# Kernel optimization log

Measured on AMD Instinct MI355X. Metric: run time of the kernel, lower is better.

Reference implementation:

```python
import jax, jax.numpy as jnp
import numpy as np

N_NODES = 50000
N_EDGES = 600000
DIM = 128
K = 3
N_LAYERS = 3
LEAKY_SLOPE = 0.01  # nn.LeakyReLU default
RE_NORM = 1.0       # 2/lambda_max with lambda_max=2 (standard ChebNet approximation)


def setup_inputs() -> dict:
    key = jax.random.key(0)
    ks = jax.random.split(key, 8)
    weights = jax.random.normal(ks[0], (N_NODES,), dtype=jnp.float32)
    src = jax.random.randint(ks[1], (N_EDGES,), 0, N_NODES)
    dst = jax.random.randint(ks[2], (N_EDGES,), 0, N_NODES)
    lin_in_w = jax.random.normal(ks[3], (1, DIM), dtype=jnp.float32) * 0.5
    lin_in_b = jnp.zeros((DIM,), dtype=jnp.float32)
    cheb_ws = jax.random.normal(ks[4], (N_LAYERS, K * DIM, DIM), dtype=jnp.float32) * 0.05
    cheb_bs = jnp.zeros((N_LAYERS, DIM), dtype=jnp.float32)
    pred_w = jax.random.normal(ks[5], (DIM, 1), dtype=jnp.float32) * 0.05
    pred_b = jnp.zeros((1,), dtype=jnp.float32)
    return {"weights": weights, "src": src, "dst": dst,
            "lin_in_w": lin_in_w, "lin_in_b": lin_in_b,
            "cheb_ws": cheb_ws, "cheb_bs": cheb_bs,
            "pred_w": pred_w, "pred_b": pred_b}


def _cheb_conv(x, W, b, src, dst, d_invsqrt, n):
    # DGL ChebConv with lambda_max=2 -> re_norm=1: scaled Laplacian L_hat = -D^-1/2 A D^-1/2
    def spmm(f):  # unnormalized Laplacian-style aggregation: D^-1/2 A D^-1/2 f
        h = f * d_invsqrt
        agg = jax.ops.segment_sum(h[src], dst, num_segments=n)
        return agg * d_invsqrt

    X0 = x
    terms = [X0]
    h = spmm(X0)
    X1 = -RE_NORM * h + X0 * (RE_NORM - 1.0)
    terms.append(X1)
    for _ in range(2, K):
        h = spmm(X1)
        Xi = -2.0 * RE_NORM * h + X1 * (2.0 * (RE_NORM - 1.0)) - X0
        terms.append(Xi)
        X0, X1 = X1, Xi
    Xt = jnp.concatenate(terms, axis=1)  # [N, K*DIM]
    return jax.nn.relu(Xt @ W + b)       # DGL ChebConv default activation=F.relu


def reference(weights, src, dst, lin_in_w, lin_in_b, cheb_ws, cheb_bs, pred_w, pred_b):
    n = weights.shape[0]
    # dgl.add_self_loop
    loop = jnp.arange(n, dtype=src.dtype)
    src_f = jnp.concatenate([src, loop])
    dst_f = jnp.concatenate([dst, loop])
    # in-degree normalization D^-1/2 (clamp min 1)
    deg = jax.ops.segment_sum(jnp.ones_like(dst_f, dtype=jnp.float32), dst_f, num_segments=n)
    d_invsqrt = jnp.power(jnp.clip(deg, 1.0), -0.5)[:, None]  # [N,1]

    feat = weights[:, None] @ lin_in_w + lin_in_b             # [N, DIM]
    emb = _cheb_conv(feat, cheb_ws[0], cheb_bs[0], src_f, dst_f, d_invsqrt, n)
    for i in range(1, N_LAYERS):
        emb = jax.nn.leaky_relu(emb, negative_slope=LEAKY_SLOPE)
        emb = _cheb_conv(emb, cheb_ws[i], cheb_bs[i], src_f, dst_f, d_invsqrt, n)
    logits = emb @ pred_w + pred_b                            # do_train=True path
    return logits
```

## Files before the change

### kernel.cpp

```cpp
#include <hip/hip_runtime.h>

typedef unsigned int uint;
typedef unsigned short ushort;

#define NN 50000
#define NE 600000
#define DIM 128
#define KD 384
#define PADK 40

typedef __attribute__((ext_vector_type(8))) short short8;
typedef __attribute__((ext_vector_type(4))) float float4v;

static __device__ __forceinline__ ushort f2b(float f) {
    uint u = __float_as_uint(f);
    return (ushort)((u + 0x7FFFu + ((u >> 16) & 1u)) >> 16);
}
static __device__ __forceinline__ float blo(uint u) { return __uint_as_float(u << 16); }
static __device__ __forceinline__ float bhi(uint u) { return __uint_as_float(u & 0xFFFF0000u); }

__global__ void k_init(int* __restrict__ cnt, const float* __restrict__ cw,
                       ushort* __restrict__ wt) {
    if (blockIdx.x < 49) {
        int i = blockIdx.x * 256 + threadIdx.x;
        if (i < 12544) ((int4*)cnt)[i] = make_int4(0, 0, 0, 0);
    } else {
        int i = (blockIdx.x - 49) * 256 + threadIdx.x;
        if (i < 3 * KD * DIM) {
            int l = i / (KD * DIM), rem = i - l * (KD * DIM);
            int k = rem >> 7, n = rem & 127;
            wt[(size_t)l * KD * DIM + (size_t)n * KD + k] = f2b(cw[i]);
        }
    }
}

__global__ void k_hist(const int* __restrict__ dst, int* __restrict__ cnt) {
    int e = blockIdx.x * 256 + threadIdx.x;
    if (e < NE) atomicAdd(&cnt[dst[e]], 1);
}

__global__ __launch_bounds__(256) void k_scan1(const int* __restrict__ cnt,
                                               int* __restrict__ incl,
                                               int* __restrict__ bsums,
                                               float* __restrict__ dinv) {
    __shared__ int sh[256];
    int i = blockIdx.x * 256 + threadIdx.x;
    int v = (i < NN) ? cnt[i] : 0;
    if (i < NN) dinv[i] = rsqrtf((float)(v + 1));
    sh[threadIdx.x] = v;
    __syncthreads();
    for (int d = 1; d < 256; d <<= 1) {
        int t = (threadIdx.x >= d) ? sh[threadIdx.x - d] : 0;
        __syncthreads();
        sh[threadIdx.x] += t;
        __syncthreads();
    }
    incl[i] = sh[threadIdx.x];
    if (threadIdx.x == 255) bsums[blockIdx.x] = sh[255];
}

__global__ __launch_bounds__(256) void k_scan3(const int* __restrict__ cnt,
                                               int* __restrict__ incl_cursor,
                                               const int* __restrict__ bsums,
                                               int* __restrict__ offs) {
    __shared__ int sh[256];
    __shared__ int boff;
    int tid = threadIdx.x;
    int v = (tid < 196) ? bsums[tid] : 0;
    sh[tid] = v;
    __syncthreads();
    for (int d = 1; d < 256; d <<= 1) {
        int t = (tid >= d) ? sh[tid - d] : 0;
        __syncthreads();
        sh[tid] += t;
        __syncthreads();
    }
    if (tid == blockIdx.x) boff = sh[tid] - v;
    __syncthreads();
    int i = blockIdx.x * 256 + tid;
    if (i >= NN) return;
    int excl = incl_cursor[i] - cnt[i] + boff;
    offs[i] = excl;
    incl_cursor[i] = excl;
    if (i == NN - 1) offs[NN] = NE;
}

__global__ void k_fill(const int* __restrict__ src, const int* __restrict__ dst,
                       int* __restrict__ cursor, const float* __restrict__ dinv,
                       const float* __restrict__ w_in,
                       uint2* __restrict__ csrE, float* __restrict__ hw) {
    int e = blockIdx.x * 256 + threadIdx.x;
    if (e < NE) {
        int s = src[e], d = dst[e];
        int p = atomicAdd(&cursor[d], 1);
        float ds = dinv[s];
        uint2 rec;
        rec.x = (uint)s;
        rec.y = __float_as_uint(ds * dinv[d]);
        csrE[p] = rec;
        hw[p] = ds * w_in[s];
    }
}

__global__ __launch_bounds__(256) void k_gather1_l1(
        const float* __restrict__ w, const float* __restrict__ lw,
        const float* __restrict__ lb, const int* __restrict__ offs,
        const uint2* __restrict__ csrE, const float* __restrict__ hw,
        const float* __restrict__ dinv,
        ushort* __restrict__ Qb, ushort* __restrict__ Pb) {
    int n = blockIdx.x * 4 + (threadIdx.x >> 6);
    int lane = threadIdx.x & 63;
    int j0 = offs[n], j1 = offs[n + 1];
    float dn = dinv[n];
    float sA = 0.f, sB = 0.f;
    const float* ew = (const float*)csrE;
    for (int j = j0 + lane; j < j1; j += 64) {
        sA += hw[j];
        sB += ew[2 * j + 1];
    }
#pragma unroll
    for (int off = 32; off > 0; off >>= 1) {
        sA += __shfl_down(sA, off, 64);
        sB += __shfl_down(sB, off, 64);
    }
    sA = __shfl(sA, 0, 64) * dn;
    sB = __shfl(sB, 0, 64);
    float id = dn * dn;
    float wn = w[n];
    float lw0 = lw[2 * lane], lw1 = lw[2 * lane + 1];
    float lb0 = lb[2 * lane], lb1 = lb[2 * lane + 1];
    float x0a = wn * lw0 + lb0, x0b = wn * lw1 + lb1;
    ushort2 pb2; pb2.x = f2b(x0a); pb2.y = f2b(x0b);
    ((ushort2*)(Pb + (size_t)n * DIM))[lane] = pb2;
    ushort2 ub;
    ub.x = f2b(-(sA * lw0 + sB * lb0 + x0a * id));
    ub.y = f2b(-(sA * lw1 + sB * lb1 + x0b * id));
    ((ushort2*)(Qb + (size_t)n * DIM))[lane] = ub;
}

__global__ __launch_bounds__(256) void k_gather1(
        const ushort* __restrict__ Xb, const int* __restrict__ offs,
        const uint2* __restrict__ csrE, const float* __restrict__ dinv,
        ushort* __restrict__ Qb) {
    int n = __builtin_amdgcn_readfirstlane(blockIdx.x * 4 + (threadIdx.x >> 6));
    int lane = threadIdx.x & 63;
    int j0 = offs[n], j1 = offs[n + 1];
    const uint* Xu = (const uint*)Xb;
    float a0 = 0.f, a1 = 0.f;
#pragma unroll 4
    for (int j = j0; j < j1; ++j) {
        uint2 e = csrE[j];
        float wv = __uint_as_float(e.y);
        uint u = Xu[(size_t)e.x * 64 + lane];
        a0 = fmaf(wv, blo(u), a0);
        a1 = fmaf(wv, bhi(u), a1);
    }
    float dn = dinv[n];
    float id = dn * dn;
    uint un = Xu[(size_t)n * 64 + lane];
    uint ow = (uint)f2b(-(a0 + blo(un) * id))
            | ((uint)f2b(-(a1 + bhi(un) * id)) << 16);
    ((uint*)Qb)[(size_t)n * 64 + lane] = ow;
}

__global__ __launch_bounds__(256) void k_gather2(
        const ushort* __restrict__ X1b, const ushort* __restrict__ X0b,
        const int* __restrict__ offs, const uint2* __restrict__ csrE,
        const float* __restrict__ dinv, ushort* __restrict__ Rb) {
    int n = __builtin_amdgcn_readfirstlane(blockIdx.x * 4 + (threadIdx.x >> 6));
    int lane = threadIdx.x & 63;
    int j0 = offs[n], j1 = offs[n + 1];
    const uint* Xu = (const uint*)X1b;
    float a0 = 0.f, a1 = 0.f;
#pragma unroll 4
    for (int j = j0; j < j1; ++j) {
        uint2 e = csrE[j];
        float wv = __uint_as_float(e.y);
        uint u = Xu[(size_t)e.x * 64 + lane];
        a0 = fmaf(wv, blo(u), a0);
        a1 = fmaf(wv, bhi(u), a1);
    }
    float dn = dinv[n];
    float id = dn * dn;
    uint u1n = Xu[(size_t)n * 64 + lane];
    uint u0n = ((const uint*)X0b)[(size_t)n * 64 + lane];
    uint ow = (uint)f2b(-2.f * (a0 + blo(u1n) * id) - blo(u0n))
            | ((uint)f2b(-2.f * (a1 + bhi(u1n) * id) - bhi(u0n)) << 16);
    ((uint*)Rb)[(size_t)n * 64 + lane] = ow;
}

__global__ __launch_bounds__(256) void k_gemm(
        const ushort* __restrict__ X0b, const ushort* __restrict__ X1b,
        const ushort* __restrict__ X2b, const ushort* __restrict__ Wt,
        const float* __restrict__ bias, ushort* __restrict__ outb) {
    __shared__ ushort As[128 * PADK];
    __shared__ ushort Bs[128 * PADK];
    int tid = threadIdx.x;
    int nbase = blockIdx.x * 128;
    int wave = tid >> 6, lane = tid & 63;
    int wr = wave >> 1, wc = wave & 1;
    int l15 = lane & 15, quad = lane >> 4;

    float4v acc[4][4];
#pragma unroll
    for (int i = 0; i < 4; ++i)
#pragma unroll
        for (int j = 0; j < 4; ++j) acc[i][j] = (float4v)0.f;

    int srow = tid >> 1, shalf = tid & 1;
    int gm = nbase + srow; if (gm >= NN) gm = NN - 1;

    for (int c = 0; c < 12; ++c) {
        int part = c >> 2;
        int k0 = (c & 3) * 32;
        const ushort* Xp = (part == 0) ? X0b : ((part == 1) ? X1b : X2b);
        const uint4* ga = (const uint4*)(Xp + (size_t)gm * DIM + k0 + shalf * 16);
        uint4 a0 = ga[0], a1 = ga[1];
        const uint4* gb = (const uint4*)(Wt + (size_t)srow * KD + c * 32 + shalf * 16);
        uint4 b0 = gb[0], b1 = gb[1];
        __syncthreads();
        uint4* pa = (uint4*)(As + srow * PADK + shalf * 16);
        pa[0] = a0; pa[1] = a1;
        uint4* pb = (uint4*)(Bs + srow * PADK + shalf * 16);
        pb[0] = b0; pb[1] = b1;
        __syncthreads();
        short8 af[4], bf[4];
#pragma unroll
        for (int i = 0; i < 4; ++i) {
            af[i] = *(const short8*)(As + (wr * 64 + i * 16 + l15) * PADK + quad * 8);
            bf[i] = *(const short8*)(Bs + (wc * 64 + i * 16 + l15) * PADK + quad * 8);
        }
#pragma unroll
        for (int i = 0; i < 4; ++i)
#pragma unroll
            for (int j = 0; j < 4; ++j)
                acc[i][j] = __builtin_amdgcn_mfma_f32_16x16x32_bf16(
                    af[i], bf[j], acc[i][j], 0, 0, 0);
    }

    float bv[4];
#pragma unroll
    for (int j = 0; j < 4; ++j) bv[j] = bias[wc * 64 + j * 16 + l15];
#pragma unroll
    for (int i = 0; i < 4; ++i) {
#pragma unroll
        for (int r = 0; r < 4; ++r) {
            int node = nbase + wr * 64 + i * 16 + quad * 4 + r;
            if (node < NN) {
#pragma unroll
                for (int j = 0; j < 4; ++j) {
                    int col = wc * 64 + j * 16 + l15;
                    outb[(size_t)node * DIM + col] =
                        f2b(fmaxf(acc[i][j][r] + bv[j], 0.f));
                }
            }
        }
    }
}

__global__ __launch_bounds__(256) void k_gemm_pred(
        const ushort* __restrict__ X0b, const ushort* __restrict__ X1b,
        const ushort* __restrict__ X2b, const ushort* __restrict__ Wt,
        const float* __restrict__ bias, const float* __restrict__ pw,
        const float* __restrict__ pb, float* __restrict__ logits) {
    __shared__ ushort As[128 * PADK];
    __shared__ ushort Bs[128 * PADK];
    __shared__ float lsum[128];
    int tid = threadIdx.x;
    int nbase = blockIdx.x * 128;
    int wave = tid >> 6, lane = tid & 63;
    int wr = wave >> 1, wc = wave & 1;
    int l15 = lane & 15, quad = lane >> 4;

    float4v acc[4][4];
#pragma unroll
    for (int i = 0; i < 4; ++i)
#pragma unroll
        for (int j = 0; j < 4; ++j) acc[i][j] = (float4v)0.f;

    int srow = tid >> 1, shalf = tid & 1;
    int gm = nbase + srow; if (gm >= NN) gm = NN - 1;

    for (int c = 0; c < 12; ++c) {
        int part = c >> 2;
        int k0 = (c & 3) * 32;
        const ushort* Xp = (part == 0) ? X0b : ((part == 1) ? X1b : X2b);
        const uint4* ga = (const uint4*)(Xp + (size_t)gm * DIM + k0 + shalf * 16);
        uint4 a0 = ga[0], a1 = ga[1];
        const uint4* gb = (const uint4*)(Wt + (size_t)srow * KD + c * 32 + shalf * 16);
        uint4 b0 = gb[0], b1 = gb[1];
        __syncthreads();
        uint4* pa = (uint4*)(As + srow * PADK + shalf * 16);
        pa[0] = a0; pa[1] = a1;
        uint4* pb2 = (uint4*)(Bs + srow * PADK + shalf * 16);
        pb2[0] = b0; pb2[1] = b1;
        __syncthreads();
        short8 af[4], bf[4];
#pragma unroll
        for (int i = 0; i < 4; ++i) {
            af[i] = *(const short8*)(As + (wr * 64 + i * 16 + l15) * PADK + quad * 8);
            bf[i] = *(const short8*)(Bs + (wc * 64 + i * 16 + l15) * PADK + quad * 8);
        }
#pragma unroll
        for (int i = 0; i < 4; ++i)
#pragma unroll
            for (int j = 0; j < 4; ++j)
                acc[i][j] = __builtin_amdgcn_mfma_f32_16x16x32_bf16(
                    af[i], bf[j], acc[i][j], 0, 0, 0);
    }

    __syncthreads();
    if (tid < 128) lsum[tid] = 0.f;
    __syncthreads();
    float bv[4], pwv[4];
#pragma unroll
    for (int j = 0; j < 4; ++j) {
        int col = wc * 64 + j * 16 + l15;
        bv[j] = bias[col];
        pwv[j] = pw[col];
    }
#pragma unroll
    for (int i = 0; i < 4; ++i) {
#pragma unroll
        for (int r = 0; r < 4; ++r) {
            float local = 0.f;
#pragma unroll
            for (int j = 0; j < 4; ++j)
                local = fmaf(fmaxf(acc[i][j][r] + bv[j], 0.f), pwv[j], local);
            local += __shfl_xor(local, 1, 64);
            local += __shfl_xor(local, 2, 64);
            local += __shfl_xor(local, 4, 64);
            local += __shfl_xor(local, 8, 64);
            if (l15 == 0)
                atomicAdd(&lsum[wr * 64 + i * 16 + quad * 4 + r], local);
        }
    }
    __syncthreads();
    if (tid < 128) {
        int node = nbase + tid;
        if (node < NN) logits[node] = lsum[tid] + pb[0];
    }
}

extern "C" void kernel_launch(void* const* d_in, const int* in_sizes, int n_in,
                              void* d_out, int out_size, void* d_ws, size_t ws_size,
                              hipStream_t stream) {
    int i_weights = 0, i_src = 1, i_dst = 2, i_lw = 3, i_lb = 4,
        i_cw = 5, i_cb = 6, i_pw = 7, i_pb = 8;
    {
        int seen600k = 0, seen128 = 0;
        for (int i = 0; i < n_in; ++i) {
            int s = in_sizes[i];
            if (s == 50000) i_weights = i;
            else if (s == 600000) { if (seen600k == 0) i_src = i; else i_dst = i; ++seen600k; }
            else if (s == 128) { if (seen128 == 0) i_lw = i; else if (seen128 == 1) i_lb = i; else i_pw = i; ++seen128; }
            else if (s == 147456) i_cw = i;
            else if (s == 384) i_cb = i;
            else if (s == 1) i_pb = i;
        }
    }
    const float* weights = (const float*)d_in[i_weights];
    const int*   src     = (const int*)d_in[i_src];
    const int*   dst     = (const int*)d_in[i_dst];
    const float* lin_w   = (const float*)d_in[i_lw];
    const float* lin_b   = (const float*)d_in[i_lb];
    const float* cheb_w  = (const float*)d_in[i_cw];
    const float* cheb_b  = (const float*)d_in[i_cb];
    const float* pred_w  = (const float*)d_in[i_pw];
    const float* pred_b  = (const float*)d_in[i_pb];
    float* out = (float*)d_out;

    float*  ws      = (float*)d_ws;
    float*  dinv    = ws;
    int*    offs    = (int*)(ws + 50048);
    int*    cnt     = offs + 50056;
    int*    incl    = cnt + 50176;
    int*    bsums   = incl + 50176;
    uint2*  csrE    = (uint2*)(bsums + 256);
    float*  hw      = (float*)(csrE + NE);
    ushort* Pb      = (ushort*)(hw + NE);
    ushort* Qb      = Pb + (size_t)NN * DIM;
    ushort* Rb      = Qb + (size_t)NN * DIM;
    ushort* Wtb     = Rb + (size_t)NN * DIM;

    k_init<<<625, 256, 0, stream>>>(cnt, cheb_w, Wtb);
    k_hist<<<2344, 256, 0, stream>>>(dst, cnt);
    k_scan1<<<196, 256, 0, stream>>>(cnt, incl, bsums, dinv);
    k_scan3<<<196, 256, 0, stream>>>(cnt, incl, bsums, offs);
    k_fill<<<2344, 256, 0, stream>>>(src, dst, incl, dinv, weights, csrE, hw);

    k_gather1_l1<<<12500, 256, 0, stream>>>(weights, lin_w, lin_b, offs, csrE,
                                            hw, dinv, Qb, Pb);
    k_gather2<<<12500, 256, 0, stream>>>(Qb, Pb, offs, csrE, dinv, Rb);
    k_gemm<<<391, 256, 0, stream>>>(Pb, Qb, Rb, Wtb, cheb_b, Pb);
    k_gather1<<<12500, 256, 0, stream>>>(Pb, offs, csrE, dinv, Qb);
    k_gather2<<<12500, 256, 0, stream>>>(Qb, Pb, offs, csrE, dinv, Rb);
    k_gemm<<<391, 256, 0, stream>>>(Pb, Qb, Rb, Wtb + (size_t)KD * DIM,
                                    cheb_b + DIM, Pb);
    k_gather1<<<12500, 256, 0, stream>>>(Pb, offs, csrE, dinv, Qb);
    k_gather2<<<12500, 256, 0, stream>>>(Qb, Pb, offs, csrE, dinv, Rb);
    k_gemm_pred<<<391, 256, 0, stream>>>(Pb, Qb, Rb, Wtb + (size_t)2 * KD * DIM,
                                         cheb_b + 2 * DIM, pred_w, pred_b, out);
}
```

Before: 361.9 us.

## Collapse first Cheb layer to rank-2 scalar propagation with precomputed weight projections

The first layer's input is rank-2 (weights times lin_w plus lin_b), so every Chebyshev term is a linear combination of lin_w and lin_b. The change propagates only two scalars per node through two sparse matrix-vector passes, precomputes the projections of lin_w and lin_b through each block of the layer-1 weights, and then forms layer-1 output with a few FMAs per element. This removes a 128-wide gather pass and a full GEMM for layer 1. In exchange it adds small extra kernels, including a single-block projection kernel, and computes layer 1 in fp32 instead of from bf16-rounded intermediates, which changes rounding slightly.

```diff
diff --git a/kernel.cpp b/kernel.cpp
--- a/kernel.cpp
+++ b/kernel.cpp
@@ -102,40 +102,102 @@
     }
 }
 
-__global__ __launch_bounds__(256) void k_gather1_l1(
-        const float* __restrict__ w, const float* __restrict__ lw,
-        const float* __restrict__ lb, const int* __restrict__ offs,
-        const uint2* __restrict__ csrE, const float* __restrict__ hw,
-        const float* __restrict__ dinv,
-        ushort* __restrict__ Qb, ushort* __restrict__ Pb) {
-    int n = blockIdx.x * 4 + (threadIdx.x >> 6);
-    int lane = threadIdx.x & 63;
+__global__ __launch_bounds__(256) void k_uv(
+        const float* __restrict__ lw, const float* __restrict__ lb,
+        const float* __restrict__ cw, float* __restrict__ uv) {
+    __shared__ float swv[128], sbv[128];
+    int tid = threadIdx.x;
+    if (tid < 128) { swv[tid] = lw[tid]; sbv[tid] = lb[tid]; }
+    __syncthreads();
+    for (int idx = tid; idx < 768; idx += 256) {
+        int vec = idx >> 7, c = idx & 127;
+        int t = vec >> 1;
+        const float* coef = (vec & 1) ? sbv : swv;
+        float s = 0.f;
+        for (int k = 0; k < 128; ++k)
+            s += coef[k] * cw[(size_t)(t * 128 + k) * 128 + c];
+        uv[idx] = s;
+    }
+}
+
+__global__ __launch_bounds__(256) void k_spmv1(
+        const int* __restrict__ offs, const uint2* __restrict__ csrE,
+        const float* __restrict__ hw, const float* __restrict__ dinv,
+        const float* __restrict__ w, float2* __restrict__ SS) {
+    int n = blockIdx.x * 16 + (threadIdx.x >> 4);
+    int l = threadIdx.x & 15;
     int j0 = offs[n], j1 = offs[n + 1];
-    float dn = dinv[n];
     float sA = 0.f, sB = 0.f;
     const float* ew = (const float*)csrE;
-    for (int j = j0 + lane; j < j1; j += 64) {
+    for (int j = j0 + l; j < j1; j += 16) {
         sA += hw[j];
         sB += ew[2 * j + 1];
     }
 #pragma unroll
-    for (int off = 32; off > 0; off >>= 1) {
-        sA += __shfl_down(sA, off, 64);
-        sB += __shfl_down(sB, off, 64);
-    }
-    sA = __shfl(sA, 0, 64) * dn;
-    sB = __shfl(sB, 0, 64);
-    float id = dn * dn;
-    float wn = w[n];
-    float lw0 = lw[2 * lane], lw1 = lw[2 * lane + 1];
-    float lb0 = lb[2 * lane], lb1 = lb[2 * lane + 1];
-    float x0a = wn * lw0 + lb0, x0b = wn * lw1 + lb1;
-    ushort2 pb2; pb2.x = f2b(x0a); pb2.y = f2b(x0b);
-    ((ushort2*)(Pb + (size_t)n * DIM))[lane] = pb2;
-    ushort2 ub;
-    ub.x = f2b(-(sA * lw0 + sB * lb0 + x0a * id));
-    ub.y = f2b(-(sA * lw1 + sB * lb1 + x0b * id));
-    ((ushort2*)(Qb + (size_t)n * DIM))[lane] = ub;
+    for (int off = 8; off > 0; off >>= 1) {
+        sA += __shfl_down(sA, off, 16);
+        sB += __shfl_down(sB, off, 16);
+    }
+    if (l == 0) {
+        float dn = dinv[n], id = dn * dn;
+        float2 o;
+        o.x = dn * sA + id * w[n];
+        o.y = sB + id;
+        SS[n] = o;
+    }
+}
+
+__global__ __launch_bounds__(256) void k_spmv2(
+        const int* __restrict__ offs, const uint2* __restrict__ csrE,
+        const float2* __restrict__ SS, const float* __restrict__ dinv,
+        float2* __restrict__ SS2) {
+    int n = blockIdx.x * 16 + (threadIdx.x >> 4);
+    int l = threadIdx.x & 15;
+    int j0 = offs[n], j1 = offs[n + 1];
+    float sC = 0.f, sD = 0.f;
+    for (int j = j0 + l; j < j1; j += 16) {
+        uint2 e = csrE[j];
+        float wv = __uint_as_float(e.y);
+        float2 s = SS[e.x];
+        sC = fmaf(wv, s.x, sC);
+        sD = fmaf(wv, s.y, sD);
+    }
+#pragma unroll
+    for (int off = 8; off > 0; off >>= 1) {
+        sC += __shfl_down(sC, off, 16);
+        sD += __shfl_down(sD, off, 16);
+    }
+    if (l == 0) {
+        float dn = dinv[n], id = dn * dn;
+        float2 s = SS[n];
+        float2 o;
+        o.x = sC + id * s.x;
+        o.y = sD + id * s.y;
+        SS2[n] = o;
+    }
+}
+
+__global__ __launch_bounds__(256) void k_l1out(
+        const float* __restrict__ w, const float2* __restrict__ SS,
+        const float2* __restrict__ SS2, const float* __restrict__ uv,
+        const float* __restrict__ bias, ushort* __restrict__ Pb) {
+    int n = blockIdx.x * 4 + (threadIdx.x >> 6);
+    int l = threadIdx.x & 63;
+    float a0 = w[n];
+    float2 s1 = SS[n], s2 = SS2[n];
+    float a1 = -s1.x, b1 = -s1.y;
+    float a2 = 2.f * s2.x - a0, b2 = 2.f * s2.y - 1.f;
+    const float2* uv2 = (const float2*)uv;
+    float2 u0 = uv2[l],       v0 = uv2[64 + l];
+    float2 u1 = uv2[128 + l], v1 = uv2[192 + l];
+    float2 u2 = uv2[256 + l], v2 = uv2[320 + l];
+    float2 bb = ((const float2*)bias)[l];
+    float o0 = bb.x + a0 * u0.x + v0.x + a1 * u1.x + b1 * v1.x + a2 * u2.x + b2 * v2.x;
+    float o1 = bb.y + a0 * u0.y + v0.y + a1 * u1.y + b1 * v1.y + a2 * u2.y + b2 * v2.y;
+    ushort2 o;
+    o.x = f2b(fmaxf(o0, 0.f));
+    o.y = f2b(fmaxf(o1, 0.f));
+    ((ushort2*)(Pb + (size_t)n * DIM))[l] = o;
 }
 
 __global__ __launch_bounds__(256) void k_gather1(
@@ -378,7 +440,10 @@
     int*    bsums   = incl + 50176;
     uint2*  csrE    = (uint2*)(bsums + 256);
     float*  hw      = (float*)(csrE + NE);
-    ushort* Pb      = (ushort*)(hw + NE);
+    float2* SS      = (float2*)(hw + NE);
+    float2* SS2     = SS + 50048;
+    float*  uv      = (float*)(SS2 + 50048);
+    ushort* Pb      = (ushort*)(uv + 768);
     ushort* Qb      = Pb + (size_t)NN * DIM;
     ushort* Rb      = Qb + (size_t)NN * DIM;
     ushort* Wtb     = Rb + (size_t)NN * DIM;
@@ -389,10 +454,11 @@
     k_scan3<<<196, 256, 0, stream>>>(cnt, incl, bsums, offs);
     k_fill<<<2344, 256, 0, stream>>>(src, dst, incl, dinv, weights, csrE, hw);
 
-    k_gather1_l1<<<12500, 256, 0, stream>>>(weights, lin_w, lin_b, offs, csrE,
-                                            hw, dinv, Qb, Pb);
-    k_gather2<<<12500, 256, 0, stream>>>(Qb, Pb, offs, csrE, dinv, Rb);
-    k_gemm<<<391, 256, 0, stream>>>(Pb, Qb, Rb, Wtb, cheb_b, Pb);
+    k_uv<<<1, 256, 0, stream>>>(lin_w, lin_b, cheb_w, uv);
+    k_spmv1<<<3125, 256, 0, stream>>>(offs, csrE, hw, dinv, weights, SS);
+    k_spmv2<<<3125, 256, 0, stream>>>(offs, csrE, SS, dinv, SS2);
+    k_l1out<<<12500, 256, 0, stream>>>(weights, SS, SS2, uv, cheb_b, Pb);
+
     k_gather1<<<12500, 256, 0, stream>>>(Pb, offs, csrE, dinv, Qb);
     k_gather2<<<12500, 256, 0, stream>>>(Qb, Pb, offs, csrE, dinv, Rb);
     k_gemm<<<391, 256, 0, stream>>>(Pb, Qb, Rb, Wtb + (size_t)KD * DIM,
```

Result: faster. 342.0 us (-5.5%).
